# Optimization experiments

Hardware: AMD Instinct MI355X
Metric: run time of the kernel (lower is better)

## Reference

```python
import jax, jax.numpy as jnp
import numpy as np

N_NODES = 800_000
N_FRAGS = 100_000
N_ROOTS = 2_000
NODE_FEATS = 86
HIDDEN = 128
MAX_BROKEN = 6
OUT_DIM = MAX_BROKEN * 2 + 1  # 13
MLP_IN = HIDDEN * 3 + OUT_DIM  # 397


def _lin_init(key, fan_in, fan_out):
    k1, k2 = jax.random.split(key)
    bound = 1.0 / np.sqrt(fan_in)
    W = jax.random.uniform(k1, (fan_in, fan_out), jnp.float32, -bound, bound)
    b = jax.random.uniform(k2, (fan_out,), jnp.float32, -bound, bound)
    return W, b


def setup_inputs() -> dict:
    key = jax.random.key(0)
    ks = jax.random.split(key, 16)
    node_h = jax.random.normal(ks[0], (N_NODES, NODE_FEATS), jnp.float32)
    segment_ids = jnp.sort(jax.random.randint(ks[1], (N_NODES,), 0, N_FRAGS))
    root_repr = jax.random.normal(ks[2], (N_ROOTS, NODE_FEATS), jnp.float32)
    ind_maps = jax.random.randint(ks[3], (N_FRAGS,), 0, N_ROOTS)
    broken = jax.random.randint(ks[4], (N_FRAGS,), 0, OUT_DIM)
    W_root, b_root = _lin_init(ks[5], NODE_FEATS, HIDDEN)
    W_in, b_in = _lin_init(ks[6], NODE_FEATS, HIDDEN)
    W_g1, b_g1 = _lin_init(ks[7], HIDDEN, HIDDEN)
    W_g2, b_g2 = _lin_init(ks[8], HIDDEN, HIDDEN)
    W_m1, b_m1 = _lin_init(ks[9], MLP_IN, HIDDEN)
    W_m2, b_m2 = _lin_init(ks[10], HIDDEN, HIDDEN)
    W_out, b_out = _lin_init(ks[11], HIDDEN, OUT_DIM)
    W_attn, b_attn = _lin_init(ks[12], HIDDEN, OUT_DIM)
    return dict(node_h=node_h, segment_ids=segment_ids, root_repr=root_repr,
                ind_maps=ind_maps, broken=broken,
                W_root=W_root, b_root=b_root, W_in=W_in, b_in=b_in,
                W_g1=W_g1, b_g1=b_g1, W_g2=W_g2, b_g2=b_g2,
                W_m1=W_m1, b_m1=b_m1, W_m2=W_m2, b_m2=b_m2,
                W_out=W_out, b_out=b_out, W_attn=W_attn, b_attn=b_attn)


def _segment_mean(x, seg_ids, num_segments):
    sums = jax.ops.segment_sum(x, seg_ids, num_segments=num_segments)
    counts = jax.ops.segment_sum(jnp.ones((x.shape[0],), x.dtype), seg_ids,
                                 num_segments=num_segments)
    return sums / jnp.maximum(counts, 1.0)[:, None]


def reference(node_h, segment_ids, root_repr, ind_maps, broken,
              W_root, b_root, W_in, b_in, W_g1, b_g1, W_g2, b_g2,
              W_m1, b_m1, W_m2, b_m2, W_out, b_out, W_attn, b_attn):
    # root encoder: Linear + ReLU (dropout=0)
    root_emb = jax.nn.relu(root_repr @ W_root + b_root)        # [R, H]
    ext_root = root_emb[ind_maps]                              # [F, H] gather
    # node input + 2 GNN (nodewise Linear+ReLU fallback) layers
    frag_h = node_h @ W_in + b_in                              # [N, H]
    frag_h = jax.nn.relu(frag_h @ W_g1 + b_g1)
    frag_h = jax.nn.relu(frag_h @ W_g2 + b_g2)
    # ragged mean-pool per fragment graph (dgl.mean_nodes)
    avg_frags = _segment_mean(frag_h, segment_ids, N_FRAGS)    # [F, H]
    # one-hot of clamped broken-bond counts
    broken_oh = jax.nn.one_hot(jnp.clip(broken, 0, MAX_BROKEN * 2), OUT_DIM,
                               dtype=frag_h.dtype)             # [F, 13]
    cat = jnp.concatenate([ext_root, ext_root - avg_frags, avg_frags,
                           broken_oh], axis=-1)                # [F, 397]
    hidden = jax.nn.relu(jax.nn.relu(cat @ W_m1 + b_m1) @ W_m2 + b_m2)
    output = jax.nn.sigmoid(hidden @ W_out + b_out)            # [F, 13]
    attn_weights = hidden @ W_attn + b_attn                    # [F, 13]
    return output, attn_weights
```

## Files before the change

kernel.cpp:

```cpp
#include <hip/hip_runtime.h>
#include <math.h>

typedef __attribute__((ext_vector_type(8))) short short8;
typedef __attribute__((ext_vector_type(4))) float float4v;

#define AST 136
#define CST 424

__device__ __forceinline__ unsigned short f2bf(float f) {
    union { float f; unsigned u; } v; v.f = f;
    return (unsigned short)((v.u + 0x7fffu + ((v.u >> 16) & 1u)) >> 16);
}
__device__ __forceinline__ float bf2f(unsigned v) {
    union { unsigned u; float f; } x; x.u = v << 16; return x.f;
}

template<int KP>
__device__ __forceinline__ void layer2t(const unsigned short* X, int astr,
                                        const unsigned short* __restrict__ WT,
                                        const float* __restrict__ bias,
                                        int lane, int tb, float4v acc[4][2])
{
    const int col0 = lane & 15, q = lane >> 4;
#pragma unroll
    for (int t = 0; t < 2; ++t) {
        float b = bias[(tb + t) * 16 + col0];
#pragma unroll
        for (int mt = 0; mt < 4; ++mt) acc[mt][t] = (float4v){b, b, b, b};
    }
#pragma unroll
    for (int ks = 0; ks < KP; ks += 32) {
        const int k0 = ks + q * 8;
        short8 B[2];
#pragma unroll
        for (int t = 0; t < 2; ++t)
            B[t] = *(const short8*)(WT + (size_t)((tb + t) * 16 + col0) * KP + k0);
#pragma unroll
        for (int mt = 0; mt < 4; ++mt) {
            short8 A = *(const short8*)(X + (mt * 16 + col0) * astr + k0);
#pragma unroll
            for (int t = 0; t < 2; ++t)
                acc[mt][t] = __builtin_amdgcn_mfma_f32_16x16x32_bf16(A, B[t], acc[mt][t], 0, 0, 0);
        }
    }
}

__device__ __forceinline__ void store2t(float4v acc[4][2], unsigned short* Y,
                                        int lane, int tb, bool relu)
{
    const int col0 = lane & 15, q = lane >> 4;
#pragma unroll
    for (int mt = 0; mt < 4; ++mt)
#pragma unroll
        for (int t = 0; t < 2; ++t)
#pragma unroll
            for (int r = 0; r < 4; ++r) {
                float v = acc[mt][t][r];
                if (relu) v = fmaxf(v, 0.0f);
                Y[(mt * 16 + q * 4 + r) * AST + (tb + t) * 16 + col0] = f2bf(v);
            }
}

__global__ void prep_kernel(const float* __restrict__ W_in, const float* __restrict__ W_g1,
                            const float* __restrict__ W_g2, const float* __restrict__ W_m1,
                            const float* __restrict__ W_m2, const float* __restrict__ W_out,
                            const float* __restrict__ W_attn, unsigned short* __restrict__ wt)
{
    int i = blockIdx.x * 256 + threadIdx.x;
    unsigned short* WT_in = wt;
    unsigned short* WT_g1 = WT_in + 12288;
    unsigned short* WT_g2 = WT_g1 + 16384;
    unsigned short* WT_m1 = WT_g2 + 16384;
    unsigned short* WT_m2 = WT_m1 + 53248;
    unsigned short* WT_h  = WT_m2 + 16384;
    if (i < 12288) { int n = i / 96, k = i - n * 96;
        WT_in[i] = (k < 86) ? f2bf(W_in[k * 128 + n]) : 0; return; }
    i -= 12288;
    if (i < 16384) { int n = i >> 7, k = i & 127;
        WT_g1[i] = f2bf(W_g1[k * 128 + n]); return; }
    i -= 16384;
    if (i < 16384) { int n = i >> 7, k = i & 127;
        WT_g2[i] = f2bf(W_g2[k * 128 + n]); return; }
    i -= 16384;
    if (i < 53248) { int n = i / 416, k = i - n * 416;
        WT_m1[i] = (k < 397) ? f2bf(W_m1[k * 128 + n]) : 0; return; }
    i -= 53248;
    if (i < 16384) { int n = i >> 7, k = i & 127;
        WT_m2[i] = f2bf(W_m2[k * 128 + n]); return; }
    i -= 16384;
    if (i < 4096) { int n = i >> 7, k = i & 127;
        WT_h[i] = (n < 13) ? f2bf(W_out[k * 13 + n])
                           : (n < 26 ? f2bf(W_attn[k * 13 + (n - 13)]) : 0); }
}

__global__ void root_kernel(const float* __restrict__ root_repr,
                            const float* __restrict__ W_root,
                            const float* __restrict__ b_root,
                            float* __restrict__ root_emb)
{
    __shared__ float x[86];
    const int r = blockIdx.x, tid = threadIdx.x;
    if (tid < 86) x[tid] = root_repr[(size_t)r * 86 + tid];
    __syncthreads();
    float acc = b_root[tid];
    for (int k = 0; k < 86; ++k)
        acc = fmaf(x[k], W_root[k * 128 + tid], acc);
    root_emb[(size_t)r * 128 + tid] = fmaxf(acc, 0.0f);
}

__global__ __launch_bounds__(256, 4)
void node_kernel(const float* __restrict__ node_h, const int* __restrict__ seg_ids,
                 const unsigned short* __restrict__ WT_in, const float* __restrict__ b_in,
                 const unsigned short* __restrict__ WT_g1, const float* __restrict__ b_g1,
                 const unsigned short* __restrict__ WT_g2, const float* __restrict__ b_g2,
                 float* __restrict__ frag_sum, float* __restrict__ frag_cnt)
{
    __shared__ __align__(16) unsigned short X[64 * AST];
    __shared__ __align__(16) unsigned short Y[64 * AST];
    __shared__ int segs[64];
    const int tid = threadIdx.x, wv = tid >> 6, lane = tid & 63, tb = wv * 2;
    const long n0 = (long)blockIdx.x * 64;

    if (tid < 64) segs[tid] = seg_ids[n0 + tid];
    {
        const float4* src = (const float4*)(node_h + n0 * 86);
#pragma unroll
        for (int j = 0; j < 6; ++j) {
            int i4 = j * 256 + tid;
            if (i4 < 1376) {
                float4 v = src[i4];
                int e = i4 << 2;
                int n = e / 86, k = e - n * 86;
                X[n * AST + k] = f2bf(v.x);
                int e1 = e + 1; n = e1 / 86; k = e1 - n * 86; X[n * AST + k] = f2bf(v.y);
                int e2 = e + 2; n = e2 / 86; k = e2 - n * 86; X[n * AST + k] = f2bf(v.z);
                int e3 = e + 3; n = e3 / 86; k = e3 - n * 86; X[n * AST + k] = f2bf(v.w);
            }
        }
        for (int idx = tid; idx < 640; idx += 256) {
            int n = idx / 10, k = idx - n * 10;
            X[n * AST + 86 + k] = 0;
        }
    }
    __syncthreads();

    float4v acc[4][2];
    layer2t<96>(X, AST, WT_in, b_in, lane, tb, acc);
    store2t(acc, Y, lane, tb, false);
    __syncthreads();
    layer2t<128>(Y, AST, WT_g1, b_g1, lane, tb, acc);
    store2t(acc, X, lane, tb, true);
    __syncthreads();
    layer2t<128>(X, AST, WT_g2, b_g2, lane, tb, acc);
    store2t(acc, Y, lane, tb, true);
    __syncthreads();

    {
        const int col = tid & 127, half = tid >> 7, r0 = half << 5;
        const int prevSeg = (half == 1) ? segs[31] : -1;
        const int nextSeg = (half == 0) ? segs[32] : -1;
        int cur = segs[r0], runStart = r0;
        float sum = 0.f, cnt = 0.f;
        for (int n = r0; n < r0 + 32; ++n) {
            int s = segs[n];
            if (s != cur) {
                bool bnd = (runStart == r0) && (half == 0 || prevSeg == cur);
                if (bnd) atomicAdd(&frag_sum[(size_t)cur * 128 + col], sum);
                else     frag_sum[(size_t)cur * 128 + col] = sum;
                if (col == 0) {
                    if (bnd) atomicAdd(&frag_cnt[cur], cnt);
                    else     frag_cnt[cur] = cnt;
                }
                sum = 0.f; cnt = 0.f; cur = s; runStart = n;
            }
            sum += bf2f((unsigned)Y[n * AST + col]);
            cnt += 1.f;
        }
        bool bnd = ((runStart == r0) && (half == 0 || prevSeg == cur))
                   || (half == 1) || (nextSeg == cur);
        if (bnd) atomicAdd(&frag_sum[(size_t)cur * 128 + col], sum);
        else     frag_sum[(size_t)cur * 128 + col] = sum;
        if (col == 0) {
            if (bnd) atomicAdd(&frag_cnt[cur], cnt);
            else     frag_cnt[cur] = cnt;
        }
    }
}

__global__ __launch_bounds__(256, 2)
void frag_kernel(const float* __restrict__ root_emb, const float* __restrict__ frag_sum,
                 const float* __restrict__ frag_cnt, const int* __restrict__ ind_maps,
                 const int* __restrict__ broken,
                 const unsigned short* __restrict__ WT_m1, const float* __restrict__ b_m1,
                 const unsigned short* __restrict__ WT_m2, const float* __restrict__ b_m2,
                 const unsigned short* __restrict__ WT_h,
                 const float* __restrict__ b_out, const float* __restrict__ b_attn,
                 float* __restrict__ out0, float* __restrict__ out1)
{
    __shared__ __align__(16) unsigned short cat[64 * CST];
    __shared__ __align__(16) unsigned short Y[64 * AST];
    unsigned short* X2 = cat;
    const int tid = threadIdx.x, wv = tid >> 6, lane = tid & 63, tb = wv * 2;
    const int col0 = lane & 15, q = lane >> 4;
    const long f0 = (long)blockIdx.x * 64;

    {
        const int m = tid >> 2, j = tid & 3;
        int fc = (int)f0 + m; if (fc > 99999) fc = 99999;
        const int rid = ind_maps[fc];
        const float inv = 1.0f / fmaxf(frag_cnt[fc], 1.0f);
        unsigned short* row = cat + m * CST;
#pragma unroll
        for (int jj = 0; jj < 8; ++jj) {
            int k = j * 32 + jj * 4;
            float4 e = *(const float4*)(root_emb + (size_t)rid * 128 + k);
            float4 s = *(const float4*)(frag_sum + (size_t)fc * 128 + k);
            float sx = s.x * inv, sy = s.y * inv, sz = s.z * inv, sw = s.w * inv;
            row[k]     = f2bf(e.x); row[k + 1] = f2bf(e.y);
            row[k + 2] = f2bf(e.z); row[k + 3] = f2bf(e.w);
            row[128 + k]     = f2bf(e.x - sx); row[128 + k + 1] = f2bf(e.y - sy);
            row[128 + k + 2] = f2bf(e.z - sz); row[128 + k + 3] = f2bf(e.w - sw);
            row[256 + k]     = f2bf(sx); row[256 + k + 1] = f2bf(sy);
            row[256 + k + 2] = f2bf(sz); row[256 + k + 3] = f2bf(sw);
        }
        if (j == 3) {
            int b = broken[fc]; b = b < 0 ? 0 : (b > 12 ? 12 : b);
            for (int kk = 0; kk < 32; ++kk)
                row[384 + kk] = (kk == b) ? 0x3f80 : 0;
        }
    }
    __syncthreads();

    float4v acc[4][2];
    layer2t<416>(cat, CST, WT_m1, b_m1, lane, tb, acc);
    store2t(acc, Y, lane, tb, true);
    __syncthreads();
    layer2t<128>(Y, AST, WT_m2, b_m2, lane, tb, acc);
    store2t(acc, X2, lane, tb, true);
    __syncthreads();

    float4v hacc[2];
#pragma unroll
    for (int t = 0; t < 2; ++t) {
        int cc = t * 16 + col0;
        float b = cc < 13 ? b_out[cc] : (cc < 26 ? b_attn[cc - 13] : 0.0f);
        hacc[t] = (float4v){b, b, b, b};
    }
#pragma unroll
    for (int ks = 0; ks < 128; ks += 32) {
        const int k0 = ks + q * 8;
        short8 A = *(const short8*)(X2 + (wv * 16 + col0) * AST + k0);
#pragma unroll
        for (int t = 0; t < 2; ++t) {
            short8 B = *(const short8*)(WT_h + (t * 16 + col0) * 128 + k0);
            hacc[t] = __builtin_amdgcn_mfma_f32_16x16x32_bf16(A, B, hacc[t], 0, 0, 0);
        }
    }
#pragma unroll
    for (int t = 0; t < 2; ++t)
#pragma unroll
        for (int r = 0; r < 4; ++r) {
            long ff = f0 + wv * 16 + q * 4 + r;
            int cc = t * 16 + col0;
            if (ff < 100000) {
                float v = hacc[t][r];
                if (cc < 13)      out0[ff * 13 + cc] = 1.0f / (1.0f + expf(-v));
                else if (cc < 26) out1[ff * 13 + cc - 13] = v;
            }
        }
}

extern "C" void kernel_launch(void* const* d_in, const int* in_sizes, int n_in,
                              void* d_out, int out_size, void* d_ws, size_t ws_size,
                              hipStream_t stream)
{
    const float* node_h    = (const float*)d_in[0];
    const int*   seg_ids   = (const int*)d_in[1];
    const float* root_repr = (const float*)d_in[2];
    const int*   ind_maps  = (const int*)d_in[3];
    const int*   broken    = (const int*)d_in[4];
    const float* W_root = (const float*)d_in[5];  const float* b_root = (const float*)d_in[6];
    const float* W_in   = (const float*)d_in[7];  const float* b_in   = (const float*)d_in[8];
    const float* W_g1   = (const float*)d_in[9];  const float* b_g1   = (const float*)d_in[10];
    const float* W_g2   = (const float*)d_in[11]; const float* b_g2   = (const float*)d_in[12];
    const float* W_m1   = (const float*)d_in[13]; const float* b_m1   = (const float*)d_in[14];
    const float* W_m2   = (const float*)d_in[15]; const float* b_m2   = (const float*)d_in[16];
    const float* W_out  = (const float*)d_in[17]; const float* b_out  = (const float*)d_in[18];
    const float* W_attn = (const float*)d_in[19]; const float* b_attn = (const float*)d_in[20];

    char* ws = (char*)d_ws;
    float* root_emb = (float*)ws;
    float* frag_sum = (float*)(ws + 1024000);
    float* frag_cnt = (float*)(ws + 52224000);
    unsigned short* wt = (unsigned short*)(ws + 52624000);
    const unsigned short* WT_in = wt;
    const unsigned short* WT_g1 = wt + 12288;
    const unsigned short* WT_g2 = WT_g1 + 16384;
    const unsigned short* WT_m1 = WT_g2 + 16384;
    const unsigned short* WT_m2 = WT_m1 + 53248;
    const unsigned short* WT_h  = WT_m2 + 16384;

    hipMemsetAsync(frag_sum, 0, 51600000, stream);

    float* out0 = (float*)d_out;
    float* out1 = out0 + (size_t)100000 * 13;

    prep_kernel<<<464, 256, 0, stream>>>(W_in, W_g1, W_g2, W_m1, W_m2, W_out, W_attn, wt);
    root_kernel<<<2000, 128, 0, stream>>>(root_repr, W_root, b_root, root_emb);
    node_kernel<<<12500, 256, 0, stream>>>(node_h, seg_ids, WT_in, b_in,
                                           WT_g1, b_g1, WT_g2, b_g2, frag_sum, frag_cnt);
    frag_kernel<<<1563, 256, 0, stream>>>(root_emb, frag_sum, frag_cnt, ind_maps, broken,
                                          WT_m1, b_m1, WT_m2, b_m2, WT_h, b_out, b_attn,
                                          out0, out1);
}
```

Baseline: 586.7 us.

## Use 8 waves per block with 2x2 MFMA tile split across rows and columns

Doubles the block size of the node and frag kernels from 256 to 512 threads and splits each 64x128 GEMM tile into a 2x2 grid of 16x16 sub-tiles per wave, instead of giving each wave all 4 row tiles for 2 column tiles. The aim is more waves in flight to hide latency and less accumulator register pressure. The segment-sum epilogue now uses four 16-row quarters, preloading values into registers, and the output head gives each wave one 16x16 tile. In exchange, each wave reloads B fragments for only half the rows, so the ratio of global weight loads to MFMA work rises, and the segment-sum issues more boundary atomics.

```diff
diff --git a/kernel.cpp b/kernel.cpp
--- a/kernel.cpp
+++ b/kernel.cpp
@@ -16,17 +16,17 @@
 }
 
 template<int KP>
-__device__ __forceinline__ void layer2t(const unsigned short* X, int astr,
+__device__ __forceinline__ void layer22(const unsigned short* X, int astr,
                                         const unsigned short* __restrict__ WT,
                                         const float* __restrict__ bias,
-                                        int lane, int tb, float4v acc[4][2])
+                                        int lane, int mt0, int nt0, float4v acc[2][2])
 {
     const int col0 = lane & 15, q = lane >> 4;
 #pragma unroll
     for (int t = 0; t < 2; ++t) {
-        float b = bias[(tb + t) * 16 + col0];
-#pragma unroll
-        for (int mt = 0; mt < 4; ++mt) acc[mt][t] = (float4v){b, b, b, b};
+        float b = bias[(nt0 + t) * 16 + col0];
+#pragma unroll
+        for (int mt = 0; mt < 2; ++mt) acc[mt][t] = (float4v){b, b, b, b};
     }
 #pragma unroll
     for (int ks = 0; ks < KP; ks += 32) {
@@ -34,10 +34,10 @@
         short8 B[2];
 #pragma unroll
         for (int t = 0; t < 2; ++t)
-            B[t] = *(const short8*)(WT + (size_t)((tb + t) * 16 + col0) * KP + k0);
-#pragma unroll
-        for (int mt = 0; mt < 4; ++mt) {
-            short8 A = *(const short8*)(X + (mt * 16 + col0) * astr + k0);
+            B[t] = *(const short8*)(WT + (size_t)((nt0 + t) * 16 + col0) * KP + k0);
+#pragma unroll
+        for (int mt = 0; mt < 2; ++mt) {
+            short8 A = *(const short8*)(X + ((mt0 + mt) * 16 + col0) * astr + k0);
 #pragma unroll
             for (int t = 0; t < 2; ++t)
                 acc[mt][t] = __builtin_amdgcn_mfma_f32_16x16x32_bf16(A, B[t], acc[mt][t], 0, 0, 0);
@@ -45,19 +45,19 @@
     }
 }
 
-__device__ __forceinline__ void store2t(float4v acc[4][2], unsigned short* Y,
-                                        int lane, int tb, bool relu)
+__device__ __forceinline__ void store22(float4v acc[2][2], unsigned short* Y,
+                                        int lane, int mt0, int nt0, bool relu)
 {
     const int col0 = lane & 15, q = lane >> 4;
 #pragma unroll
-    for (int mt = 0; mt < 4; ++mt)
+    for (int mt = 0; mt < 2; ++mt)
 #pragma unroll
         for (int t = 0; t < 2; ++t)
 #pragma unroll
             for (int r = 0; r < 4; ++r) {
                 float v = acc[mt][t][r];
                 if (relu) v = fmaxf(v, 0.0f);
-                Y[(mt * 16 + q * 4 + r) * AST + (tb + t) * 16 + col0] = f2bf(v);
+                Y[((mt0 + mt) * 16 + q * 4 + r) * AST + (nt0 + t) * 16 + col0] = f2bf(v);
             }
 }
 
@@ -108,7 +108,7 @@
     root_emb[(size_t)r * 128 + tid] = fmaxf(acc, 0.0f);
 }
 
-__global__ __launch_bounds__(256, 4)
+__global__ __launch_bounds__(512, 8)
 void node_kernel(const float* __restrict__ node_h, const int* __restrict__ seg_ids,
                  const unsigned short* __restrict__ WT_in, const float* __restrict__ b_in,
                  const unsigned short* __restrict__ WT_g1, const float* __restrict__ b_g1,
@@ -118,15 +118,16 @@
     __shared__ __align__(16) unsigned short X[64 * AST];
     __shared__ __align__(16) unsigned short Y[64 * AST];
     __shared__ int segs[64];
-    const int tid = threadIdx.x, wv = tid >> 6, lane = tid & 63, tb = wv * 2;
+    const int tid = threadIdx.x, wv = tid >> 6, lane = tid & 63;
+    const int mt0 = (wv >> 2) * 2, nt0 = (wv & 3) * 2;
     const long n0 = (long)blockIdx.x * 64;
 
     if (tid < 64) segs[tid] = seg_ids[n0 + tid];
     {
         const float4* src = (const float4*)(node_h + n0 * 86);
 #pragma unroll
-        for (int j = 0; j < 6; ++j) {
-            int i4 = j * 256 + tid;
+        for (int j = 0; j < 3; ++j) {
+            int i4 = j * 512 + tid;
             if (i4 < 1376) {
                 float4 v = src[i4];
                 int e = i4 << 2;
@@ -137,34 +138,40 @@
                 int e3 = e + 3; n = e3 / 86; k = e3 - n * 86; X[n * AST + k] = f2bf(v.w);
             }
         }
-        for (int idx = tid; idx < 640; idx += 256) {
+        for (int idx = tid; idx < 640; idx += 512) {
             int n = idx / 10, k = idx - n * 10;
             X[n * AST + 86 + k] = 0;
         }
     }
     __syncthreads();
 
-    float4v acc[4][2];
-    layer2t<96>(X, AST, WT_in, b_in, lane, tb, acc);
-    store2t(acc, Y, lane, tb, false);
-    __syncthreads();
-    layer2t<128>(Y, AST, WT_g1, b_g1, lane, tb, acc);
-    store2t(acc, X, lane, tb, true);
-    __syncthreads();
-    layer2t<128>(X, AST, WT_g2, b_g2, lane, tb, acc);
-    store2t(acc, Y, lane, tb, true);
+    float4v acc[2][2];
+    layer22<96>(X, AST, WT_in, b_in, lane, mt0, nt0, acc);
+    store22(acc, Y, lane, mt0, nt0, false);
+    __syncthreads();
+    layer22<128>(Y, AST, WT_g1, b_g1, lane, mt0, nt0, acc);
+    store22(acc, X, lane, mt0, nt0, true);
+    __syncthreads();
+    layer22<128>(X, AST, WT_g2, b_g2, lane, mt0, nt0, acc);
+    store22(acc, Y, lane, mt0, nt0, true);
     __syncthreads();
 
     {
-        const int col = tid & 127, half = tid >> 7, r0 = half << 5;
-        const int prevSeg = (half == 1) ? segs[31] : -1;
-        const int nextSeg = (half == 0) ? segs[32] : -1;
+        const int col = tid & 127, qt = tid >> 7, r0 = qt << 4;
+        float v[16];
+#pragma unroll
+        for (int i = 0; i < 16; ++i)
+            v[i] = bf2f((unsigned)Y[(r0 + i) * AST + col]);
+        const int prevSeg = (qt > 0) ? segs[r0 - 1] : -1;
+        const int nextSeg = (qt < 3) ? segs[r0 + 16] : -1;
         int cur = segs[r0], runStart = r0;
         float sum = 0.f, cnt = 0.f;
-        for (int n = r0; n < r0 + 32; ++n) {
+#pragma unroll
+        for (int i = 0; i < 16; ++i) {
+            const int n = r0 + i;
             int s = segs[n];
             if (s != cur) {
-                bool bnd = (runStart == r0) && (half == 0 || prevSeg == cur);
+                bool bnd = (runStart == r0) && (qt == 0 || prevSeg == cur);
                 if (bnd) atomicAdd(&frag_sum[(size_t)cur * 128 + col], sum);
                 else     frag_sum[(size_t)cur * 128 + col] = sum;
                 if (col == 0) {
@@ -173,11 +180,11 @@
                 }
                 sum = 0.f; cnt = 0.f; cur = s; runStart = n;
             }
-            sum += bf2f((unsigned)Y[n * AST + col]);
+            sum += v[i];
             cnt += 1.f;
         }
-        bool bnd = ((runStart == r0) && (half == 0 || prevSeg == cur))
-                   || (half == 1) || (nextSeg == cur);
+        bool bnd = ((runStart == r0) && (qt == 0 || prevSeg == cur))
+                   || (qt == 3) || (nextSeg == cur);
         if (bnd) atomicAdd(&frag_sum[(size_t)cur * 128 + col], sum);
         else     frag_sum[(size_t)cur * 128 + col] = sum;
         if (col == 0) {
@@ -187,7 +194,7 @@
     }
 }
 
-__global__ __launch_bounds__(256, 2)
+__global__ __launch_bounds__(512, 4)
 void frag_kernel(const float* __restrict__ root_emb, const float* __restrict__ frag_sum,
                  const float* __restrict__ frag_cnt, const int* __restrict__ ind_maps,
                  const int* __restrict__ broken,
@@ -200,19 +207,20 @@
     __shared__ __align__(16) unsigned short cat[64 * CST];
     __shared__ __align__(16) unsigned short Y[64 * AST];
     unsigned short* X2 = cat;
-    const int tid = threadIdx.x, wv = tid >> 6, lane = tid & 63, tb = wv * 2;
+    const int tid = threadIdx.x, wv = tid >> 6, lane = tid & 63;
+    const int mt0 = (wv >> 2) * 2, nt0 = (wv & 3) * 2;
     const int col0 = lane & 15, q = lane >> 4;
     const long f0 = (long)blockIdx.x * 64;
 
     {
-        const int m = tid >> 2, j = tid & 3;
+        const int m = tid >> 3, j = tid & 7;
         int fc = (int)f0 + m; if (fc > 99999) fc = 99999;
         const int rid = ind_maps[fc];
         const float inv = 1.0f / fmaxf(frag_cnt[fc], 1.0f);
         unsigned short* row = cat + m * CST;
 #pragma unroll
-        for (int jj = 0; jj < 8; ++jj) {
-            int k = j * 32 + jj * 4;
+        for (int jj = 0; jj < 4; ++jj) {
+            int k = j * 16 + jj * 4;
             float4 e = *(const float4*)(root_emb + (size_t)rid * 128 + k);
             float4 s = *(const float4*)(frag_sum + (size_t)fc * 128 + k);
             float sx = s.x * inv, sy = s.y * inv, sz = s.z * inv, sw = s.w * inv;
@@ -223,7 +231,7 @@
             row[256 + k]     = f2bf(sx); row[256 + k + 1] = f2bf(sy);
             row[256 + k + 2] = f2bf(sz); row[256 + k + 3] = f2bf(sw);
         }
-        if (j == 3) {
+        if (j == 7) {
             int b = broken[fc]; b = b < 0 ? 0 : (b > 12 ? 12 : b);
             for (int kk = 0; kk < 32; ++kk)
                 row[384 + kk] = (kk == b) ? 0x3f80 : 0;
@@ -231,43 +239,36 @@
     }
     __syncthreads();
 
-    float4v acc[4][2];
-    layer2t<416>(cat, CST, WT_m1, b_m1, lane, tb, acc);
-    store2t(acc, Y, lane, tb, true);
-    __syncthreads();
-    layer2t<128>(Y, AST, WT_m2, b_m2, lane, tb, acc);
-    store2t(acc, X2, lane, tb, true);
-    __syncthreads();
-
-    float4v hacc[2];
-#pragma unroll
-    for (int t = 0; t < 2; ++t) {
-        int cc = t * 16 + col0;
+    float4v acc[2][2];
+    layer22<416>(cat, CST, WT_m1, b_m1, lane, mt0, nt0, acc);
+    store22(acc, Y, lane, mt0, nt0, true);
+    __syncthreads();
+    layer22<128>(Y, AST, WT_m2, b_m2, lane, mt0, nt0, acc);
+    store22(acc, X2, lane, mt0, nt0, true);
+    __syncthreads();
+
+    {
+        const int mrow = wv & 3, t = wv >> 2;
+        const int cc = t * 16 + col0;
         float b = cc < 13 ? b_out[cc] : (cc < 26 ? b_attn[cc - 13] : 0.0f);
-        hacc[t] = (float4v){b, b, b, b};
-    }
-#pragma unroll
-    for (int ks = 0; ks < 128; ks += 32) {
-        const int k0 = ks + q * 8;
-        short8 A = *(const short8*)(X2 + (wv * 16 + col0) * AST + k0);
-#pragma unroll
-        for (int t = 0; t < 2; ++t) {
+        float4v hacc = (float4v){b, b, b, b};
+#pragma unroll
+        for (int ks = 0; ks < 128; ks += 32) {
+            const int k0 = ks + q * 8;
+            short8 A = *(const short8*)(X2 + (mrow * 16 + col0) * AST + k0);
             short8 B = *(const short8*)(WT_h + (t * 16 + col0) * 128 + k0);
-            hacc[t] = __builtin_amdgcn_mfma_f32_16x16x32_bf16(A, B, hacc[t], 0, 0, 0);
-        }
-    }
-#pragma unroll
-    for (int t = 0; t < 2; ++t)
+            hacc = __builtin_amdgcn_mfma_f32_16x16x32_bf16(A, B, hacc, 0, 0, 0);
+        }
 #pragma unroll
         for (int r = 0; r < 4; ++r) {
-            long ff = f0 + wv * 16 + q * 4 + r;
-            int cc = t * 16 + col0;
+            long ff = f0 + mrow * 16 + q * 4 + r;
             if (ff < 100000) {
-                float v = hacc[t][r];
+                float v = hacc[r];
                 if (cc < 13)      out0[ff * 13 + cc] = 1.0f / (1.0f + expf(-v));
                 else if (cc < 26) out1[ff * 13 + cc - 13] = v;
             }
         }
+    }
 }
 
 extern "C" void kernel_launch(void* const* d_in, const int* in_sizes, int n_in,
@@ -307,9 +308,9 @@
 
     prep_kernel<<<464, 256, 0, stream>>>(W_in, W_g1, W_g2, W_m1, W_m2, W_out, W_attn, wt);
     root_kernel<<<2000, 128, 0, stream>>>(root_repr, W_root, b_root, root_emb);
-    node_kernel<<<12500, 256, 0, stream>>>(node_h, seg_ids, WT_in, b_in,
+    node_kernel<<<12500, 512, 0, stream>>>(node_h, seg_ids, WT_in, b_in,
                                            WT_g1, b_g1, WT_g2, b_g2, frag_sum, frag_cnt);
-    frag_kernel<<<1563, 256, 0, stream>>>(root_emb, frag_sum, frag_cnt, ind_maps, broken,
+    frag_kernel<<<1563, 512, 0, stream>>>(root_emb, frag_sum, frag_cnt, ind_maps, broken,
                                           WT_m1, b_m1, WT_m2, b_m2, WT_h, b_out, b_attn,
                                           out0, out1);
 }
```

After: 686.6 us. 1.17x slower.

## Swap MFMA operand order to get row-contiguous outputs and vectorize LDS stores

Applied to the files above, without the earlier changes.

Swaps the A/B operands of the bf16 MFMA so each lane's accumulator holds four consecutive output columns of one row. The epilogue can then pack four bf16 values into a single 8-byte LDS store instead of four scattered 2-byte stores. The segment-mean pooling is rebuilt so each thread sums 4 columns over 8 rows, loading them with vector LDS reads, and the concat-building writes in the fragment kernel are packed the same way. The goal is fewer LDS transactions and fewer bank conflicts, at the cost of more atomics at segment boundaries, since the node chunks per block are now finer (8 chunks of 8 rows instead of 2 of 32).

```diff
diff --git a/kernel.cpp b/kernel.cpp
--- a/kernel.cpp
+++ b/kernel.cpp
@@ -24,23 +24,23 @@
     const int col0 = lane & 15, q = lane >> 4;
 #pragma unroll
     for (int t = 0; t < 2; ++t) {
-        float b = bias[(tb + t) * 16 + col0];
-#pragma unroll
-        for (int mt = 0; mt < 4; ++mt) acc[mt][t] = (float4v){b, b, b, b};
+        const float4 b4 = *(const float4*)(bias + (tb + t) * 16 + q * 4);
+#pragma unroll
+        for (int mt = 0; mt < 4; ++mt) acc[mt][t] = (float4v){b4.x, b4.y, b4.z, b4.w};
     }
 #pragma unroll
     for (int ks = 0; ks < KP; ks += 32) {
         const int k0 = ks + q * 8;
-        short8 B[2];
+        short8 Wv[2];
 #pragma unroll
         for (int t = 0; t < 2; ++t)
-            B[t] = *(const short8*)(WT + (size_t)((tb + t) * 16 + col0) * KP + k0);
+            Wv[t] = *(const short8*)(WT + (size_t)((tb + t) * 16 + col0) * KP + k0);
 #pragma unroll
         for (int mt = 0; mt < 4; ++mt) {
-            short8 A = *(const short8*)(X + (mt * 16 + col0) * astr + k0);
+            short8 Xv = *(const short8*)(X + (mt * 16 + col0) * astr + k0);
 #pragma unroll
             for (int t = 0; t < 2; ++t)
-                acc[mt][t] = __builtin_amdgcn_mfma_f32_16x16x32_bf16(A, B[t], acc[mt][t], 0, 0, 0);
+                acc[mt][t] = __builtin_amdgcn_mfma_f32_16x16x32_bf16(Wv[t], Xv, acc[mt][t], 0, 0, 0);
         }
     }
 }
@@ -52,13 +52,18 @@
 #pragma unroll
     for (int mt = 0; mt < 4; ++mt)
 #pragma unroll
-        for (int t = 0; t < 2; ++t)
-#pragma unroll
-            for (int r = 0; r < 4; ++r) {
-                float v = acc[mt][t][r];
-                if (relu) v = fmaxf(v, 0.0f);
-                Y[(mt * 16 + q * 4 + r) * AST + (tb + t) * 16 + col0] = f2bf(v);
+        for (int t = 0; t < 2; ++t) {
+            float v0 = acc[mt][t][0], v1 = acc[mt][t][1];
+            float v2 = acc[mt][t][2], v3 = acc[mt][t][3];
+            if (relu) {
+                v0 = fmaxf(v0, 0.0f); v1 = fmaxf(v1, 0.0f);
+                v2 = fmaxf(v2, 0.0f); v3 = fmaxf(v3, 0.0f);
             }
+            uint2 w;
+            w.x = (unsigned)f2bf(v0) | ((unsigned)f2bf(v1) << 16);
+            w.y = (unsigned)f2bf(v2) | ((unsigned)f2bf(v3) << 16);
+            *(uint2*)(Y + (mt * 16 + col0) * AST + (tb + t) * 16 + q * 4) = w;
+        }
 }
 
 __global__ void prep_kernel(const float* __restrict__ W_in, const float* __restrict__ W_g1,
@@ -156,31 +161,43 @@
     __syncthreads();
 
     {
-        const int col = tid & 127, half = tid >> 7, r0 = half << 5;
-        const int prevSeg = (half == 1) ? segs[31] : -1;
-        const int nextSeg = (half == 0) ? segs[32] : -1;
+        const int cg = tid & 31, oct = tid >> 5;
+        const int col = cg * 4, r0 = oct * 8;
+        ushort4 raw[8];
+#pragma unroll
+        for (int i = 0; i < 8; ++i)
+            raw[i] = *(const ushort4*)(Y + (r0 + i) * AST + col);
+        const int prevSeg = (oct > 0) ? segs[r0 - 1] : -1;
+        const int nextSeg = (oct < 7) ? segs[r0 + 8] : -1;
         int cur = segs[r0], runStart = r0;
-        float sum = 0.f, cnt = 0.f;
-        for (int n = r0; n < r0 + 32; ++n) {
-            int s = segs[n];
-            if (s != cur) {
-                bool bnd = (runStart == r0) && (half == 0 || prevSeg == cur);
-                if (bnd) atomicAdd(&frag_sum[(size_t)cur * 128 + col], sum);
-                else     frag_sum[(size_t)cur * 128 + col] = sum;
-                if (col == 0) {
+        float s0 = 0.f, s1 = 0.f, s2 = 0.f, s3 = 0.f, cnt = 0.f;
+#pragma unroll
+        for (int i = 0; i < 8; ++i) {
+            const int n = r0 + i;
+            int sg = segs[n];
+            if (sg != cur) {
+                bool bnd = (runStart == r0) && (oct == 0 || prevSeg == cur);
+                float* dst = &frag_sum[(size_t)cur * 128 + col];
+                if (bnd) { atomicAdd(dst, s0); atomicAdd(dst + 1, s1);
+                           atomicAdd(dst + 2, s2); atomicAdd(dst + 3, s3); }
+                else     { dst[0] = s0; dst[1] = s1; dst[2] = s2; dst[3] = s3; }
+                if (cg == 0) {
                     if (bnd) atomicAdd(&frag_cnt[cur], cnt);
                     else     frag_cnt[cur] = cnt;
                 }
-                sum = 0.f; cnt = 0.f; cur = s; runStart = n;
+                s0 = s1 = s2 = s3 = 0.f; cnt = 0.f; cur = sg; runStart = n;
             }
-            sum += bf2f((unsigned)Y[n * AST + col]);
+            s0 += bf2f(raw[i].x); s1 += bf2f(raw[i].y);
+            s2 += bf2f(raw[i].z); s3 += bf2f(raw[i].w);
             cnt += 1.f;
         }
-        bool bnd = ((runStart == r0) && (half == 0 || prevSeg == cur))
-                   || (half == 1) || (nextSeg == cur);
-        if (bnd) atomicAdd(&frag_sum[(size_t)cur * 128 + col], sum);
-        else     frag_sum[(size_t)cur * 128 + col] = sum;
-        if (col == 0) {
+        bool bnd = ((runStart == r0) && (oct == 0 || prevSeg == cur))
+                   || (oct == 7) || (nextSeg == cur);
+        float* dst = &frag_sum[(size_t)cur * 128 + col];
+        if (bnd) { atomicAdd(dst, s0); atomicAdd(dst + 1, s1);
+                   atomicAdd(dst + 2, s2); atomicAdd(dst + 3, s3); }
+        else     { dst[0] = s0; dst[1] = s1; dst[2] = s2; dst[3] = s3; }
+        if (cg == 0) {
             if (bnd) atomicAdd(&frag_cnt[cur], cnt);
             else     frag_cnt[cur] = cnt;
         }
@@ -216,17 +233,26 @@
             float4 e = *(const float4*)(root_emb + (size_t)rid * 128 + k);
             float4 s = *(const float4*)(frag_sum + (size_t)fc * 128 + k);
             float sx = s.x * inv, sy = s.y * inv, sz = s.z * inv, sw = s.w * inv;
-            row[k]     = f2bf(e.x); row[k + 1] = f2bf(e.y);
-            row[k + 2] = f2bf(e.z); row[k + 3] = f2bf(e.w);
-            row[128 + k]     = f2bf(e.x - sx); row[128 + k + 1] = f2bf(e.y - sy);
-            row[128 + k + 2] = f2bf(e.z - sz); row[128 + k + 3] = f2bf(e.w - sw);
-            row[256 + k]     = f2bf(sx); row[256 + k + 1] = f2bf(sy);
-            row[256 + k + 2] = f2bf(sz); row[256 + k + 3] = f2bf(sw);
+            uint2 w;
+            w.x = (unsigned)f2bf(e.x) | ((unsigned)f2bf(e.y) << 16);
+            w.y = (unsigned)f2bf(e.z) | ((unsigned)f2bf(e.w) << 16);
+            *(uint2*)(row + k) = w;
+            w.x = (unsigned)f2bf(e.x - sx) | ((unsigned)f2bf(e.y - sy) << 16);
+            w.y = (unsigned)f2bf(e.z - sz) | ((unsigned)f2bf(e.w - sw) << 16);
+            *(uint2*)(row + 128 + k) = w;
+            w.x = (unsigned)f2bf(sx) | ((unsigned)f2bf(sy) << 16);
+            w.y = (unsigned)f2bf(sz) | ((unsigned)f2bf(sw) << 16);
+            *(uint2*)(row + 256 + k) = w;
         }
         if (j == 3) {
             int b = broken[fc]; b = b < 0 ? 0 : (b > 12 ? 12 : b);
-            for (int kk = 0; kk < 32; ++kk)
-                row[384 + kk] = (kk == b) ? 0x3f80 : 0;
+#pragma unroll
+            for (int kk = 0; kk < 32; kk += 4) {
+                uint2 w;
+                w.x = ((kk     == b) ? 0x3f80u : 0u) | (((kk + 1 == b) ? 0x3f80u : 0u) << 16);
+                w.y = ((kk + 2 == b) ? 0x3f80u : 0u) | (((kk + 3 == b) ? 0x3f80u : 0u) << 16);
+                *(uint2*)(row + 384 + kk) = w;
+            }
         }
     }
     __syncthreads();
@@ -242,32 +268,37 @@
     float4v hacc[2];
 #pragma unroll
     for (int t = 0; t < 2; ++t) {
-        int cc = t * 16 + col0;
-        float b = cc < 13 ? b_out[cc] : (cc < 26 ? b_attn[cc - 13] : 0.0f);
-        hacc[t] = (float4v){b, b, b, b};
+        const int cc0 = t * 16 + q * 4;
+#pragma unroll
+        for (int r = 0; r < 4; ++r) {
+            int c = cc0 + r;
+            hacc[t][r] = c < 13 ? b_out[c] : (c < 26 ? b_attn[c - 13] : 0.0f);
+        }
     }
 #pragma unroll
     for (int ks = 0; ks < 128; ks += 32) {
         const int k0 = ks + q * 8;
-        short8 A = *(const short8*)(X2 + (wv * 16 + col0) * AST + k0);
+        short8 Xv = *(const short8*)(X2 + (wv * 16 + col0) * AST + k0);
 #pragma unroll
         for (int t = 0; t < 2; ++t) {
-            short8 B = *(const short8*)(WT_h + (t * 16 + col0) * 128 + k0);
-            hacc[t] = __builtin_amdgcn_mfma_f32_16x16x32_bf16(A, B, hacc[t], 0, 0, 0);
-        }
-    }
-#pragma unroll
-    for (int t = 0; t < 2; ++t)
-#pragma unroll
-        for (int r = 0; r < 4; ++r) {
-            long ff = f0 + wv * 16 + q * 4 + r;
-            int cc = t * 16 + col0;
-            if (ff < 100000) {
-                float v = hacc[t][r];
-                if (cc < 13)      out0[ff * 13 + cc] = 1.0f / (1.0f + expf(-v));
-                else if (cc < 26) out1[ff * 13 + cc - 13] = v;
-            }
-        }
+            short8 Hv = *(const short8*)(WT_h + (t * 16 + col0) * 128 + k0);
+            hacc[t] = __builtin_amdgcn_mfma_f32_16x16x32_bf16(Hv, Xv, hacc[t], 0, 0, 0);
+        }
+    }
+    {
+        const long ff = f0 + wv * 16 + col0;
+        if (ff < 100000) {
+#pragma unroll
+            for (int t = 0; t < 2; ++t)
+#pragma unroll
+                for (int r = 0; r < 4; ++r) {
+                    int cc = t * 16 + q * 4 + r;
+                    float v = hacc[t][r];
+                    if (cc < 13)      out0[ff * 13 + cc] = 1.0f / (1.0f + expf(-v));
+                    else if (cc < 26) out1[ff * 13 + cc - 13] = v;
+                }
+        }
+    }
 }
 
 extern "C" void kernel_launch(void* const* d_in, const int* in_sizes, int n_in,
```

New measurement: 737.0 us. +25.6%, slower.

## Prefetch layer weights into registers and halve frag tile for higher occupancy

Applied to the files above, without the earlier changes.

In node_kernel, each layer's weight fragments are loaded into registers before the preceding store and barrier, so the global weight loads overlap the node_h staging and the LDS stores. frag_kernel now processes 32 fragments per block instead of 64, which halves its LDS footprint and raises launch bounds and grid size. It also packs cat writes into 64-bit stores and splits the output head across the four waves. The cost is more registers held for the prefetched weights, which could limit occupancy in node_kernel.

```diff
diff --git a/kernel.cpp b/kernel.cpp
--- a/kernel.cpp
+++ b/kernel.cpp
@@ -16,17 +16,56 @@
 }
 
 template<int KP>
-__device__ __forceinline__ void layer2t(const unsigned short* X, int astr,
-                                        const unsigned short* __restrict__ WT,
-                                        const float* __restrict__ bias,
-                                        int lane, int tb, float4v acc[4][2])
+__device__ __forceinline__ void loadW(const unsigned short* __restrict__ WT,
+                                      int lane, int tb, short8 Wv[2][KP / 32])
+{
+    const int col0 = lane & 15, q = lane >> 4;
+#pragma unroll
+    for (int t = 0; t < 2; ++t)
+#pragma unroll
+        for (int ksi = 0; ksi < KP / 32; ++ksi)
+            Wv[t][ksi] = *(const short8*)(WT + (size_t)((tb + t) * 16 + col0) * KP
+                                          + ksi * 32 + q * 8);
+}
+
+template<int KP, int MT>
+__device__ __forceinline__ void layerP(const unsigned short* X, int astr,
+                                       const float* __restrict__ bias,
+                                       int lane, int tb,
+                                       const short8 Wv[2][KP / 32], float4v acc[MT][2])
 {
     const int col0 = lane & 15, q = lane >> 4;
 #pragma unroll
     for (int t = 0; t < 2; ++t) {
         float b = bias[(tb + t) * 16 + col0];
 #pragma unroll
-        for (int mt = 0; mt < 4; ++mt) acc[mt][t] = (float4v){b, b, b, b};
+        for (int mt = 0; mt < MT; ++mt) acc[mt][t] = (float4v){b, b, b, b};
+    }
+#pragma unroll
+    for (int ksi = 0; ksi < KP / 32; ++ksi) {
+        const int k0 = ksi * 32 + q * 8;
+#pragma unroll
+        for (int mt = 0; mt < MT; ++mt) {
+            short8 A = *(const short8*)(X + (mt * 16 + col0) * astr + k0);
+#pragma unroll
+            for (int t = 0; t < 2; ++t)
+                acc[mt][t] = __builtin_amdgcn_mfma_f32_16x16x32_bf16(A, Wv[t][ksi], acc[mt][t], 0, 0, 0);
+        }
+    }
+}
+
+template<int KP, int MT>
+__device__ __forceinline__ void layerG(const unsigned short* X, int astr,
+                                       const unsigned short* __restrict__ WT,
+                                       const float* __restrict__ bias,
+                                       int lane, int tb, float4v acc[MT][2])
+{
+    const int col0 = lane & 15, q = lane >> 4;
+#pragma unroll
+    for (int t = 0; t < 2; ++t) {
+        float b = bias[(tb + t) * 16 + col0];
+#pragma unroll
+        for (int mt = 0; mt < MT; ++mt) acc[mt][t] = (float4v){b, b, b, b};
     }
 #pragma unroll
     for (int ks = 0; ks < KP; ks += 32) {
@@ -36,7 +75,7 @@
         for (int t = 0; t < 2; ++t)
             B[t] = *(const short8*)(WT + (size_t)((tb + t) * 16 + col0) * KP + k0);
 #pragma unroll
-        for (int mt = 0; mt < 4; ++mt) {
+        for (int mt = 0; mt < MT; ++mt) {
             short8 A = *(const short8*)(X + (mt * 16 + col0) * astr + k0);
 #pragma unroll
             for (int t = 0; t < 2; ++t)
@@ -45,12 +84,13 @@
     }
 }
 
-__device__ __forceinline__ void store2t(float4v acc[4][2], unsigned short* Y,
-                                        int lane, int tb, bool relu)
-{
-    const int col0 = lane & 15, q = lane >> 4;
-#pragma unroll
-    for (int mt = 0; mt < 4; ++mt)
+template<int MT>
+__device__ __forceinline__ void storeP(float4v acc[MT][2], unsigned short* Y,
+                                       int lane, int tb, bool relu)
+{
+    const int col0 = lane & 15, q = lane >> 4;
+#pragma unroll
+    for (int mt = 0; mt < MT; ++mt)
 #pragma unroll
         for (int t = 0; t < 2; ++t)
 #pragma unroll
@@ -121,6 +161,9 @@
     const int tid = threadIdx.x, wv = tid >> 6, lane = tid & 63, tb = wv * 2;
     const long n0 = (long)blockIdx.x * 64;
 
+    short8 W1[2][3];
+    loadW<96>(WT_in, lane, tb, W1);
+
     if (tid < 64) segs[tid] = seg_ids[n0 + tid];
     {
         const float4* src = (const float4*)(node_h + n0 * 86);
@@ -145,14 +188,18 @@
     __syncthreads();
 
     float4v acc[4][2];
-    layer2t<96>(X, AST, WT_in, b_in, lane, tb, acc);
-    store2t(acc, Y, lane, tb, false);
-    __syncthreads();
-    layer2t<128>(Y, AST, WT_g1, b_g1, lane, tb, acc);
-    store2t(acc, X, lane, tb, true);
-    __syncthreads();
-    layer2t<128>(X, AST, WT_g2, b_g2, lane, tb, acc);
-    store2t(acc, Y, lane, tb, true);
+    layerP<96, 4>(X, AST, b_in, lane, tb, W1, acc);
+    short8 W2[2][4];
+    loadW<128>(WT_g1, lane, tb, W2);
+    storeP<4>(acc, Y, lane, tb, false);
+    __syncthreads();
+    layerP<128, 4>(Y, AST, b_g1, lane, tb, W2, acc);
+    short8 W3[2][4];
+    loadW<128>(WT_g2, lane, tb, W3);
+    storeP<4>(acc, X, lane, tb, true);
+    __syncthreads();
+    layerP<128, 4>(X, AST, b_g2, lane, tb, W3, acc);
+    storeP<4>(acc, Y, lane, tb, true);
     __syncthreads();
 
     {
@@ -187,7 +234,7 @@
     }
 }
 
-__global__ __launch_bounds__(256, 2)
+__global__ __launch_bounds__(256, 4)
 void frag_kernel(const float* __restrict__ root_emb, const float* __restrict__ frag_sum,
                  const float* __restrict__ frag_cnt, const int* __restrict__ ind_maps,
                  const int* __restrict__ broken,
@@ -197,77 +244,83 @@
                  const float* __restrict__ b_out, const float* __restrict__ b_attn,
                  float* __restrict__ out0, float* __restrict__ out1)
 {
-    __shared__ __align__(16) unsigned short cat[64 * CST];
-    __shared__ __align__(16) unsigned short Y[64 * AST];
+    __shared__ __align__(16) unsigned short cat[32 * CST];
+    __shared__ __align__(16) unsigned short Y[32 * AST];
     unsigned short* X2 = cat;
     const int tid = threadIdx.x, wv = tid >> 6, lane = tid & 63, tb = wv * 2;
     const int col0 = lane & 15, q = lane >> 4;
-    const long f0 = (long)blockIdx.x * 64;
+    const long f0 = (long)blockIdx.x * 32;
 
     {
-        const int m = tid >> 2, j = tid & 3;
+        const int m = tid >> 3, j = tid & 7;
         int fc = (int)f0 + m; if (fc > 99999) fc = 99999;
         const int rid = ind_maps[fc];
         const float inv = 1.0f / fmaxf(frag_cnt[fc], 1.0f);
         unsigned short* row = cat + m * CST;
 #pragma unroll
-        for (int jj = 0; jj < 8; ++jj) {
-            int k = j * 32 + jj * 4;
+        for (int jj = 0; jj < 4; ++jj) {
+            int k = j * 16 + jj * 4;
             float4 e = *(const float4*)(root_emb + (size_t)rid * 128 + k);
             float4 s = *(const float4*)(frag_sum + (size_t)fc * 128 + k);
             float sx = s.x * inv, sy = s.y * inv, sz = s.z * inv, sw = s.w * inv;
-            row[k]     = f2bf(e.x); row[k + 1] = f2bf(e.y);
-            row[k + 2] = f2bf(e.z); row[k + 3] = f2bf(e.w);
-            row[128 + k]     = f2bf(e.x - sx); row[128 + k + 1] = f2bf(e.y - sy);
-            row[128 + k + 2] = f2bf(e.z - sz); row[128 + k + 3] = f2bf(e.w - sw);
-            row[256 + k]     = f2bf(sx); row[256 + k + 1] = f2bf(sy);
-            row[256 + k + 2] = f2bf(sz); row[256 + k + 3] = f2bf(sw);
-        }
-        if (j == 3) {
+            uint2 w;
+            w.x = (unsigned)f2bf(e.x) | ((unsigned)f2bf(e.y) << 16);
+            w.y = (unsigned)f2bf(e.z) | ((unsigned)f2bf(e.w) << 16);
+            *(uint2*)(row + k) = w;
+            w.x = (unsigned)f2bf(e.x - sx) | ((unsigned)f2bf(e.y - sy) << 16);
+            w.y = (unsigned)f2bf(e.z - sz) | ((unsigned)f2bf(e.w - sw) << 16);
+            *(uint2*)(row + 128 + k) = w;
+            w.x = (unsigned)f2bf(sx) | ((unsigned)f2bf(sy) << 16);
+            w.y = (unsigned)f2bf(sz) | ((unsigned)f2bf(sw) << 16);
+            *(uint2*)(row + 256 + k) = w;
+        }
+        if (j == 7) {
             int b = broken[fc]; b = b < 0 ? 0 : (b > 12 ? 12 : b);
-            for (int kk = 0; kk < 32; ++kk)
-                row[384 + kk] = (kk == b) ? 0x3f80 : 0;
-        }
-    }
-    __syncthreads();
-
-    float4v acc[4][2];
-    layer2t<416>(cat, CST, WT_m1, b_m1, lane, tb, acc);
-    store2t(acc, Y, lane, tb, true);
-    __syncthreads();
-    layer2t<128>(Y, AST, WT_m2, b_m2, lane, tb, acc);
-    store2t(acc, X2, lane, tb, true);
-    __syncthreads();
-
-    float4v hacc[2];
-#pragma unroll
-    for (int t = 0; t < 2; ++t) {
-        int cc = t * 16 + col0;
+#pragma unroll
+            for (int kk = 0; kk < 32; kk += 4) {
+                uint2 w;
+                w.x = ((kk     == b) ? 0x3f80u : 0u) | (((kk + 1 == b) ? 0x3f80u : 0u) << 16);
+                w.y = ((kk + 2 == b) ? 0x3f80u : 0u) | (((kk + 3 == b) ? 0x3f80u : 0u) << 16);
+                *(uint2*)(row + 384 + kk) = w;
+            }
+        }
+    }
+    __syncthreads();
+
+    float4v acc[2][2];
+    layerG<416, 2>(cat, CST, WT_m1, b_m1, lane, tb, acc);
+    short8 Wm2[2][4];
+    loadW<128>(WT_m2, lane, tb, Wm2);
+    storeP<2>(acc, Y, lane, tb, true);
+    __syncthreads();
+    layerP<128, 2>(Y, AST, b_m2, lane, tb, Wm2, acc);
+    const int mrow = wv & 1, t_h = wv >> 1;
+    short8 Wh[4];
+#pragma unroll
+    for (int ksi = 0; ksi < 4; ++ksi)
+        Wh[ksi] = *(const short8*)(WT_h + (t_h * 16 + col0) * 128 + ksi * 32 + q * 8);
+    storeP<2>(acc, X2, lane, tb, true);
+    __syncthreads();
+
+    {
+        const int cc = t_h * 16 + col0;
         float b = cc < 13 ? b_out[cc] : (cc < 26 ? b_attn[cc - 13] : 0.0f);
-        hacc[t] = (float4v){b, b, b, b};
-    }
-#pragma unroll
-    for (int ks = 0; ks < 128; ks += 32) {
-        const int k0 = ks + q * 8;
-        short8 A = *(const short8*)(X2 + (wv * 16 + col0) * AST + k0);
-#pragma unroll
-        for (int t = 0; t < 2; ++t) {
-            short8 B = *(const short8*)(WT_h + (t * 16 + col0) * 128 + k0);
-            hacc[t] = __builtin_amdgcn_mfma_f32_16x16x32_bf16(A, B, hacc[t], 0, 0, 0);
-        }
-    }
-#pragma unroll
-    for (int t = 0; t < 2; ++t)
+        float4v hacc = (float4v){b, b, b, b};
+#pragma unroll
+        for (int ksi = 0; ksi < 4; ++ksi) {
+            short8 A = *(const short8*)(X2 + (mrow * 16 + col0) * AST + ksi * 32 + q * 8);
+            hacc = __builtin_amdgcn_mfma_f32_16x16x32_bf16(A, Wh[ksi], hacc, 0, 0, 0);
+        }
 #pragma unroll
         for (int r = 0; r < 4; ++r) {
-            long ff = f0 + wv * 16 + q * 4 + r;
-            int cc = t * 16 + col0;
+            long ff = f0 + mrow * 16 + q * 4 + r;
             if (ff < 100000) {
-                float v = hacc[t][r];
+                float v = hacc[r];
                 if (cc < 13)      out0[ff * 13 + cc] = 1.0f / (1.0f + expf(-v));
                 else if (cc < 26) out1[ff * 13 + cc - 13] = v;
             }
         }
+    }
 }
 
 extern "C" void kernel_launch(void* const* d_in, const int* in_sizes, int n_in,
@@ -309,7 +362,7 @@
     root_kernel<<<2000, 128, 0, stream>>>(root_repr, W_root, b_root, root_emb);
     node_kernel<<<12500, 256, 0, stream>>>(node_h, seg_ids, WT_in, b_in,
                                            WT_g1, b_g1, WT_g2, b_g2, frag_sum, frag_cnt);
-    frag_kernel<<<1563, 256, 0, stream>>>(root_emb, frag_sum, frag_cnt, ind_maps, broken,
+    frag_kernel<<<3125, 256, 0, stream>>>(root_emb, frag_sum, frag_cnt, ind_maps, broken,
                                           WT_m1, b_m1, WT_m2, b_m2, WT_h, b_out, b_attn,
                                           out0, out1);
 }
```

Measured after the change: 591.2 us. Within noise of the previous version (+0.8%).
